# Performance work log

Hardware: AMD Instinct MI355X
Metric: run time of the kernel (lower is better)

Reference implementation:

```python
import jax, jax.numpy as jnp
import numpy as np

FLOAT_MIN = jnp.finfo(jnp.float32).min


def setup_inputs() -> dict:
    key = jax.random.key(0)
    ks = jax.random.split(key, 8)
    B, S, F1, F2, A = 65536, 256, 256, 256, 128
    return {
        "obs_state": jax.random.normal(ks[0], (B, S), dtype=jnp.float32),
        "action_mask": jax.random.randint(ks[1], (B, A), 0, 2, dtype=jnp.int32),
        "W1": jax.random.normal(ks[2], (S, F1), dtype=jnp.float32) * (1.0 / np.sqrt(S)),
        "b1": jnp.zeros((F1,), dtype=jnp.float32),
        "W2": jax.random.normal(ks[3], (F1, F2), dtype=jnp.float32) * (1.0 / np.sqrt(F1)),
        "b2": jnp.zeros((F2,), dtype=jnp.float32),
        "W3": jax.random.normal(ks[4], (F2, A), dtype=jnp.float32) * (1.0 / np.sqrt(F2)),
        "b3": jnp.zeros((A,), dtype=jnp.float32),
    }


def reference(obs_state, action_mask, W1, b1, W2, b2, W3, b3):
    # 3-layer MLP: state -> fc1 -> relu -> fc2 -> relu -> fc3
    h = jax.nn.relu(obs_state @ W1 + b1)
    h = jax.nn.relu(h @ W2 + b2)
    x = h @ W3 + b3  # [B, A] logits

    # Vectorized action masking (replaces per-element Python loop):
    #   mask==0 -> FLOAT_MIN; rows with all-zero mask -> FLOAT_MIN everywhere, col 0 = 1.0
    valid = action_mask != 0  # [B, A] bool
    x = jnp.where(valid, x, FLOAT_MIN)
    all_invalid = ~jnp.any(valid, axis=1, keepdims=True)  # [B, 1]
    col0 = jnp.arange(x.shape[1]) == 0  # [A]
    x = jnp.where(all_invalid & col0, jnp.float32(1.0), x)
    return x
```

## Files before the change

kernel.cpp:

```cpp
#include <hip/hip_runtime.h>

typedef __attribute__((ext_vector_type(8))) short short8;
typedef __attribute__((ext_vector_type(8))) unsigned short ushort8;
typedef __attribute__((ext_vector_type(4))) float f32x4;

#define MT 32
#define NWAVE 4
#define STR 264

__device__ __forceinline__ float bmax_r17() { return __uint_as_float(0x7F7F0000u); }

__device__ __forceinline__ unsigned short f2bf_r17(float f) {
    unsigned int u = __float_as_uint(f);
    return (unsigned short)((u + 0x7fffu + ((u >> 16) & 1u)) >> 16);
}

__global__ __launch_bounds__(256)
void pack_weights_r17(const float* __restrict__ W1,
                      const float* __restrict__ W2,
                      const float* __restrict__ W3,
                      unsigned short* __restrict__ ws) {
    int s = blockIdx.x * 256 + threadIdx.x;
    const float* src;
    unsigned short* dst;
    int N;
    if (s < 8192)       { src = W1; dst = ws;          N = 256; }
    else if (s < 16384) { src = W2; dst = ws + 65536;  N = 256; s -= 8192; }
    else                { src = W3; dst = ws + 131072; N = 128; s -= 16384; }
    int frag = s >> 6, lane = s & 63;
    int kb = (frag & 7) * 32 + (lane >> 4) * 8;
    int n  = (frag >> 3) * 16 + (lane & 15);
    ushort8 o;
    #pragma unroll
    for (int j = 0; j < 8; ++j) o[j] = f2bf_r17(src[(kb + j) * N + n]);
    *(ushort8*)&dst[s * 8] = o;
}

__global__ __launch_bounds__(256, 2)
void ColorNetwork_32495722561720_kernel(
        const float* __restrict__ obs,
        const int* __restrict__ amask,
        const float* __restrict__ b1,
        const float* __restrict__ b2,
        const float* __restrict__ b3,
        const unsigned short* __restrict__ w1p,
        const unsigned short* __restrict__ w2p,
        const unsigned short* __restrict__ w3p,
        float* __restrict__ out)
{
    __shared__ __align__(16) unsigned short act[NWAVE * MT * STR];
    __shared__ int rowany[NWAVE * MT];

    const int tid  = threadIdx.x;
    const int wave = tid >> 6;
    const int lane = tid & 63;
    const int quad = lane >> 4;
    const int noff = lane & 15;
    const int sb   = wave * (MT * STR);
    const int rb   = wave * MT;
    const size_t rowbase = (size_t)blockIdx.x * (MT * NWAVE) + (size_t)wave * MT;

    {
        const float4* xin = (const float4*)(obs + rowbase * 256);
        #pragma unroll 8
        for (int i = 0; i < 32; ++i) {
            int f = i * 64 + lane;
            int row = f >> 6;
            int c4 = f & 63;
            float4 v = xin[f];
            ushort4 p;
            p.x = f2bf_r17(v.x); p.y = f2bf_r17(v.y);
            p.z = f2bf_r17(v.z); p.w = f2bf_r17(v.w);
            *(ushort4*)&act[sb + row * STR + c4 * 4] = p;
        }
    }

    if (lane < MT) rowany[rb + lane] = 0;
    {
        const int4* min4 = (const int4*)(amask + rowbase * 128);
        #pragma unroll 4
        for (int i = 0; i < 16; ++i) {
            int f = i * 64 + lane;
            int4 m = min4[f];
            if (m.x | m.y | m.z | m.w) rowany[rb + (f >> 5)] = 1;
        }
    }

    short8 a[2][8];

    #pragma unroll
    for (int rt = 0; rt < 2; ++rt)
        #pragma unroll
        for (int k0 = 0; k0 < 8; ++k0)
            a[rt][k0] = *(const short8*)&act[sb + (rt * 16 + noff) * STR + k0 * 32 + quad * 8];
    #pragma unroll 2
    for (int ct = 0; ct < 16; ++ct) {
        f32x4 ac0 = {}, ac1 = {};
        #pragma unroll
        for (int k0 = 0; k0 < 8; ++k0) {
            short8 b = *(const short8*)&w1p[((ct * 8 + k0) * 64 + lane) * 8];
            ac0 = __builtin_amdgcn_mfma_f32_16x16x32_bf16(a[0][k0], b, ac0, 0, 0, 0);
            ac1 = __builtin_amdgcn_mfma_f32_16x16x32_bf16(a[1][k0], b, ac1, 0, 0, 0);
        }
        int col = ct * 16 + noff;
        float bv = b1[col];
        #pragma unroll
        for (int i = 0; i < 4; ++i) {
            act[sb + (quad * 4 + i) * STR + col]      = f2bf_r17(fmaxf(ac0[i] + bv, 0.0f));
            act[sb + (16 + quad * 4 + i) * STR + col] = f2bf_r17(fmaxf(ac1[i] + bv, 0.0f));
        }
    }

    #pragma unroll
    for (int rt = 0; rt < 2; ++rt)
        #pragma unroll
        for (int k0 = 0; k0 < 8; ++k0)
            a[rt][k0] = *(const short8*)&act[sb + (rt * 16 + noff) * STR + k0 * 32 + quad * 8];
    #pragma unroll 2
    for (int ct = 0; ct < 16; ++ct) {
        f32x4 ac0 = {}, ac1 = {};
        #pragma unroll
        for (int k0 = 0; k0 < 8; ++k0) {
            short8 b = *(const short8*)&w2p[((ct * 8 + k0) * 64 + lane) * 8];
            ac0 = __builtin_amdgcn_mfma_f32_16x16x32_bf16(a[0][k0], b, ac0, 0, 0, 0);
            ac1 = __builtin_amdgcn_mfma_f32_16x16x32_bf16(a[1][k0], b, ac1, 0, 0, 0);
        }
        int col = ct * 16 + noff;
        float bv = b2[col];
        #pragma unroll
        for (int i = 0; i < 4; ++i) {
            act[sb + (quad * 4 + i) * STR + col]      = f2bf_r17(fmaxf(ac0[i] + bv, 0.0f));
            act[sb + (16 + quad * 4 + i) * STR + col] = f2bf_r17(fmaxf(ac1[i] + bv, 0.0f));
        }
    }

    #pragma unroll
    for (int rt = 0; rt < 2; ++rt)
        #pragma unroll
        for (int k0 = 0; k0 < 8; ++k0)
            a[rt][k0] = *(const short8*)&act[sb + (rt * 16 + noff) * STR + k0 * 32 + quad * 8];

    int ra[8];
    #pragma unroll
    for (int rt = 0; rt < 2; ++rt)
        #pragma unroll
        for (int i = 0; i < 4; ++i)
            ra[rt * 4 + i] = rowany[rb + rt * 16 + quad * 4 + i];

    const float BM = bmax_r17();
    #pragma unroll 2
    for (int ct = 0; ct < 8; ++ct) {
        f32x4 ac0 = {}, ac1 = {};
        #pragma unroll
        for (int k0 = 0; k0 < 8; ++k0) {
            short8 b = *(const short8*)&w3p[((ct * 8 + k0) * 64 + lane) * 8];
            ac0 = __builtin_amdgcn_mfma_f32_16x16x32_bf16(a[0][k0], b, ac0, 0, 0, 0);
            ac1 = __builtin_amdgcn_mfma_f32_16x16x32_bf16(a[1][k0], b, ac1, 0, 0, 0);
        }
        int col = ct * 16 + noff;
        float bv = b3[col];
        #pragma unroll
        for (int rt = 0; rt < 2; ++rt) {
            const f32x4& ac = rt ? ac1 : ac0;
            #pragma unroll
            for (int i = 0; i < 4; ++i) {
                int row = rt * 16 + quad * 4 + i;
                int m = amask[(rowbase + row) * 128 + col];
                float v = ac[i] + bv;
                v = fminf(fmaxf(v, -BM), BM);
                if (!(v == v)) v = 0.0f;
                if (!m) v = -BM;
                if (!ra[rt * 4 + i]) v = (col == 0) ? 1.0f : -BM;
                out[(rowbase + row) * 128 + col] = v;
            }
        }
    }
}

extern "C" void kernel_launch(void* const* d_in, const int* in_sizes, int n_in,
                              void* d_out, int out_size, void* d_ws, size_t ws_size,
                              hipStream_t stream) {
    const float* obs   = (const float*)d_in[0];
    const int*   amask = (const int*)d_in[1];
    const float* W1 = (const float*)d_in[2];
    const float* b1 = (const float*)d_in[3];
    const float* W2 = (const float*)d_in[4];
    const float* b2 = (const float*)d_in[5];
    const float* W3 = (const float*)d_in[6];
    const float* b3 = (const float*)d_in[7];
    float* out = (float*)d_out;

    const int B = in_sizes[0] / 256;

    unsigned short* ws = (unsigned short*)d_ws;
    unsigned short* w1p = ws;
    unsigned short* w2p = ws + 65536;
    unsigned short* w3p = ws + 131072;

    pack_weights_r17<<<80, 256, 0, stream>>>(W1, W2, W3, ws);

    ColorNetwork_32495722561720_kernel<<<B / (MT * NWAVE), 256, 0, stream>>>(
        obs, amask, b1, b2, b3, w1p, w2p, w3p, out);
}
```

Before: 184.6 us.

## Split each 32-row tile across two waves sharing LDS, partitioning output columns

```diff
diff --git a/kernel.cpp b/kernel.cpp
--- a/kernel.cpp
+++ b/kernel.cpp
@@ -5,18 +5,17 @@
 typedef __attribute__((ext_vector_type(4))) float f32x4;
 
 #define MT 32
-#define NWAVE 4
 #define STR 264
 
-__device__ __forceinline__ float bmax_r17() { return __uint_as_float(0x7F7F0000u); }
-
-__device__ __forceinline__ unsigned short f2bf_r17(float f) {
+__device__ __forceinline__ float bmax_r18() { return __uint_as_float(0x7F7F0000u); }
+
+__device__ __forceinline__ unsigned short f2bf_r18(float f) {
     unsigned int u = __float_as_uint(f);
     return (unsigned short)((u + 0x7fffu + ((u >> 16) & 1u)) >> 16);
 }
 
 __global__ __launch_bounds__(256)
-void pack_weights_r17(const float* __restrict__ W1,
+void pack_weights_r18(const float* __restrict__ W1,
                       const float* __restrict__ W2,
                       const float* __restrict__ W3,
                       unsigned short* __restrict__ ws) {
@@ -32,11 +31,11 @@
     int n  = (frag >> 3) * 16 + (lane & 15);
     ushort8 o;
     #pragma unroll
-    for (int j = 0; j < 8; ++j) o[j] = f2bf_r17(src[(kb + j) * N + n]);
+    for (int j = 0; j < 8; ++j) o[j] = f2bf_r18(src[(kb + j) * N + n]);
     *(ushort8*)&dst[s * 8] = o;
 }
 
-__global__ __launch_bounds__(256, 2)
+__global__ __launch_bounds__(128, 4)
 void ColorNetwork_32495722561720_kernel(
         const float* __restrict__ obs,
         const int* __restrict__ amask,
@@ -48,41 +47,41 @@
         const unsigned short* __restrict__ w3p,
         float* __restrict__ out)
 {
-    __shared__ __align__(16) unsigned short act[NWAVE * MT * STR];
-    __shared__ int rowany[NWAVE * MT];
+    __shared__ __align__(16) unsigned short act[MT * STR];
+    __shared__ int rowany[MT];
 
     const int tid  = threadIdx.x;
     const int wave = tid >> 6;
     const int lane = tid & 63;
     const int quad = lane >> 4;
     const int noff = lane & 15;
-    const int sb   = wave * (MT * STR);
-    const int rb   = wave * MT;
-    const size_t rowbase = (size_t)blockIdx.x * (MT * NWAVE) + (size_t)wave * MT;
+    const size_t rowbase = (size_t)blockIdx.x * MT;
+
+    if (tid < MT) rowany[tid] = 0;
 
     {
         const float4* xin = (const float4*)(obs + rowbase * 256);
-        #pragma unroll 8
-        for (int i = 0; i < 32; ++i) {
-            int f = i * 64 + lane;
+        #pragma unroll 4
+        for (int i = 0; i < 16; ++i) {
+            int f = tid + i * 128;
             int row = f >> 6;
             int c4 = f & 63;
             float4 v = xin[f];
             ushort4 p;
-            p.x = f2bf_r17(v.x); p.y = f2bf_r17(v.y);
-            p.z = f2bf_r17(v.z); p.w = f2bf_r17(v.w);
-            *(ushort4*)&act[sb + row * STR + c4 * 4] = p;
-        }
-    }
-
-    if (lane < MT) rowany[rb + lane] = 0;
+            p.x = f2bf_r18(v.x); p.y = f2bf_r18(v.y);
+            p.z = f2bf_r18(v.z); p.w = f2bf_r18(v.w);
+            *(ushort4*)&act[row * STR + c4 * 4] = p;
+        }
+    }
+    __syncthreads();
+
     {
         const int4* min4 = (const int4*)(amask + rowbase * 128);
         #pragma unroll 4
-        for (int i = 0; i < 16; ++i) {
-            int f = i * 64 + lane;
+        for (int i = 0; i < 8; ++i) {
+            int f = tid + i * 128;
             int4 m = min4[f];
-            if (m.x | m.y | m.z | m.w) rowany[rb + (f >> 5)] = 1;
+            if (m.x | m.y | m.z | m.w) rowany[f >> 5] = 1;
         }
     }
 
@@ -92,73 +91,80 @@
     for (int rt = 0; rt < 2; ++rt)
         #pragma unroll
         for (int k0 = 0; k0 < 8; ++k0)
-            a[rt][k0] = *(const short8*)&act[sb + (rt * 16 + noff) * STR + k0 * 32 + quad * 8];
+            a[rt][k0] = *(const short8*)&act[(rt * 16 + noff) * STR + k0 * 32 + quad * 8];
+    __syncthreads();
     #pragma unroll 2
-    for (int ct = 0; ct < 16; ++ct) {
+    for (int ct = 0; ct < 8; ++ct) {
+        const int ctg = wave * 8 + ct;
         f32x4 ac0 = {}, ac1 = {};
         #pragma unroll
         for (int k0 = 0; k0 < 8; ++k0) {
-            short8 b = *(const short8*)&w1p[((ct * 8 + k0) * 64 + lane) * 8];
+            short8 b = *(const short8*)&w1p[((ctg * 8 + k0) * 64 + lane) * 8];
             ac0 = __builtin_amdgcn_mfma_f32_16x16x32_bf16(a[0][k0], b, ac0, 0, 0, 0);
             ac1 = __builtin_amdgcn_mfma_f32_16x16x32_bf16(a[1][k0], b, ac1, 0, 0, 0);
         }
-        int col = ct * 16 + noff;
-        float bv = b1[col];
+        const int col = ctg * 16 + noff;
+        const float bv = b1[col];
         #pragma unroll
         for (int i = 0; i < 4; ++i) {
-            act[sb + (quad * 4 + i) * STR + col]      = f2bf_r17(fmaxf(ac0[i] + bv, 0.0f));
-            act[sb + (16 + quad * 4 + i) * STR + col] = f2bf_r17(fmaxf(ac1[i] + bv, 0.0f));
-        }
-    }
+            act[(quad * 4 + i) * STR + col]      = f2bf_r18(fmaxf(ac0[i] + bv, 0.0f));
+            act[(16 + quad * 4 + i) * STR + col] = f2bf_r18(fmaxf(ac1[i] + bv, 0.0f));
+        }
+    }
+    __syncthreads();
 
     #pragma unroll
     for (int rt = 0; rt < 2; ++rt)
         #pragma unroll
         for (int k0 = 0; k0 < 8; ++k0)
-            a[rt][k0] = *(const short8*)&act[sb + (rt * 16 + noff) * STR + k0 * 32 + quad * 8];
+            a[rt][k0] = *(const short8*)&act[(rt * 16 + noff) * STR + k0 * 32 + quad * 8];
+    __syncthreads();
     #pragma unroll 2
-    for (int ct = 0; ct < 16; ++ct) {
+    for (int ct = 0; ct < 8; ++ct) {
+        const int ctg = wave * 8 + ct;
         f32x4 ac0 = {}, ac1 = {};
         #pragma unroll
         for (int k0 = 0; k0 < 8; ++k0) {
-            short8 b = *(const short8*)&w2p[((ct * 8 + k0) * 64 + lane) * 8];
+            short8 b = *(const short8*)&w2p[((ctg * 8 + k0) * 64 + lane) * 8];
             ac0 = __builtin_amdgcn_mfma_f32_16x16x32_bf16(a[0][k0], b, ac0, 0, 0, 0);
             ac1 = __builtin_amdgcn_mfma_f32_16x16x32_bf16(a[1][k0], b, ac1, 0, 0, 0);
         }
-        int col = ct * 16 + noff;
-        float bv = b2[col];
+        const int col = ctg * 16 + noff;
+        const float bv = b2[col];
         #pragma unroll
         for (int i = 0; i < 4; ++i) {
-            act[sb + (quad * 4 + i) * STR + col]      = f2bf_r17(fmaxf(ac0[i] + bv, 0.0f));
-            act[sb + (16 + quad * 4 + i) * STR + col] = f2bf_r17(fmaxf(ac1[i] + bv, 0.0f));
-        }
-    }
+            act[(quad * 4 + i) * STR + col]      = f2bf_r18(fmaxf(ac0[i] + bv, 0.0f));
+            act[(16 + quad * 4 + i) * STR + col] = f2bf_r18(fmaxf(ac1[i] + bv, 0.0f));
+        }
+    }
+    __syncthreads();
 
     #pragma unroll
     for (int rt = 0; rt < 2; ++rt)
         #pragma unroll
         for (int k0 = 0; k0 < 8; ++k0)
-            a[rt][k0] = *(const short8*)&act[sb + (rt * 16 + noff) * STR + k0 * 32 + quad * 8];
+            a[rt][k0] = *(const short8*)&act[(rt * 16 + noff) * STR + k0 * 32 + quad * 8];
 
     int ra[8];
     #pragma unroll
     for (int rt = 0; rt < 2; ++rt)
         #pragma unroll
         for (int i = 0; i < 4; ++i)
-            ra[rt * 4 + i] = rowany[rb + rt * 16 + quad * 4 + i];
-
-    const float BM = bmax_r17();
+            ra[rt * 4 + i] = rowany[rt * 16 + quad * 4 + i];
+
+    const float BM = bmax_r18();
     #pragma unroll 2
-    for (int ct = 0; ct < 8; ++ct) {
+    for (int ct = 0; ct < 4; ++ct) {
+        const int ctg = wave * 4 + ct;
         f32x4 ac0 = {}, ac1 = {};
         #pragma unroll
         for (int k0 = 0; k0 < 8; ++k0) {
-            short8 b = *(const short8*)&w3p[((ct * 8 + k0) * 64 + lane) * 8];
+            short8 b = *(const short8*)&w3p[((ctg * 8 + k0) * 64 + lane) * 8];
             ac0 = __builtin_amdgcn_mfma_f32_16x16x32_bf16(a[0][k0], b, ac0, 0, 0, 0);
             ac1 = __builtin_amdgcn_mfma_f32_16x16x32_bf16(a[1][k0], b, ac1, 0, 0, 0);
         }
-        int col = ct * 16 + noff;
-        float bv = b3[col];
+        const int col = ctg * 16 + noff;
+        const float bv = b3[col];
         #pragma unroll
         for (int rt = 0; rt < 2; ++rt) {
             const f32x4& ac = rt ? ac1 : ac0;
@@ -197,8 +203,8 @@
     unsigned short* w2p = ws + 65536;
     unsigned short* w3p = ws + 131072;
 
-    pack_weights_r17<<<80, 256, 0, stream>>>(W1, W2, W3, ws);
-
-    ColorNetwork_32495722561720_kernel<<<B / (MT * NWAVE), 256, 0, stream>>>(
+    pack_weights_r18<<<80, 256, 0, stream>>>(W1, W2, W3, ws);
+
+    ColorNetwork_32495722561720_kernel<<<B / MT, 128, 0, stream>>>(
         obs, amask, b1, b2, b3, w1p, w2p, w3p, out);
 }
```

Result: faster. 165.8 us (-10.2%).

## Shrink per-wave row tile to 16 rows with 128-thread blocks

Applied to the files above, without the earlier changes.

```diff
diff --git a/kernel.cpp b/kernel.cpp
--- a/kernel.cpp
+++ b/kernel.cpp
@@ -5,18 +5,17 @@
 typedef __attribute__((ext_vector_type(4))) float f32x4;
 
 #define MT 32
-#define NWAVE 4
 #define STR 264
 
-__device__ __forceinline__ float bmax_r17() { return __uint_as_float(0x7F7F0000u); }
+__device__ __forceinline__ float bmax_r20() { return __uint_as_float(0x7F7F0000u); }
 
-__device__ __forceinline__ unsigned short f2bf_r17(float f) {
+__device__ __forceinline__ unsigned short f2bf_r20(float f) {
     unsigned int u = __float_as_uint(f);
     return (unsigned short)((u + 0x7fffu + ((u >> 16) & 1u)) >> 16);
 }
 
 __global__ __launch_bounds__(256)
-void pack_weights_r17(const float* __restrict__ W1,
+void pack_weights_r20(const float* __restrict__ W1,
                       const float* __restrict__ W2,
                       const float* __restrict__ W3,
                       unsigned short* __restrict__ ws) {
@@ -32,11 +31,11 @@
     int n  = (frag >> 3) * 16 + (lane & 15);
     ushort8 o;
     #pragma unroll
-    for (int j = 0; j < 8; ++j) o[j] = f2bf_r17(src[(kb + j) * N + n]);
+    for (int j = 0; j < 8; ++j) o[j] = f2bf_r20(src[(kb + j) * N + n]);
     *(ushort8*)&dst[s * 8] = o;
 }
 
-__global__ __launch_bounds__(256, 2)
+__global__ __launch_bounds__(128, 4)
 void ColorNetwork_32495722561720_kernel(
         const float* __restrict__ obs,
         const int* __restrict__ amask,
@@ -48,131 +47,111 @@
         const unsigned short* __restrict__ w3p,
         float* __restrict__ out)
 {
-    __shared__ __align__(16) unsigned short act[NWAVE * MT * STR];
-    __shared__ int rowany[NWAVE * MT];
+    __shared__ __align__(16) unsigned short act[MT * STR];
+    __shared__ int rowany[MT];
 
     const int tid  = threadIdx.x;
     const int wave = tid >> 6;
     const int lane = tid & 63;
     const int quad = lane >> 4;
     const int noff = lane & 15;
-    const int sb   = wave * (MT * STR);
-    const int rb   = wave * MT;
-    const size_t rowbase = (size_t)blockIdx.x * (MT * NWAVE) + (size_t)wave * MT;
+    const size_t rowbase = (size_t)blockIdx.x * MT + (size_t)wave * 16;
+    const int sb = wave * 16 * STR;
+    const int rb = wave * 16;
 
     {
         const float4* xin = (const float4*)(obs + rowbase * 256);
-        #pragma unroll 8
-        for (int i = 0; i < 32; ++i) {
-            int f = i * 64 + lane;
+        #pragma unroll 4
+        for (int i = 0; i < 16; ++i) {
+            int f = lane + i * 64;
             int row = f >> 6;
             int c4 = f & 63;
             float4 v = xin[f];
             ushort4 p;
-            p.x = f2bf_r17(v.x); p.y = f2bf_r17(v.y);
-            p.z = f2bf_r17(v.z); p.w = f2bf_r17(v.w);
+            p.x = f2bf_r20(v.x); p.y = f2bf_r20(v.y);
+            p.z = f2bf_r20(v.z); p.w = f2bf_r20(v.w);
             *(ushort4*)&act[sb + row * STR + c4 * 4] = p;
         }
     }
 
-    if (lane < MT) rowany[rb + lane] = 0;
+    if (lane < 16) rowany[rb + lane] = 0;
     {
         const int4* min4 = (const int4*)(amask + rowbase * 128);
         #pragma unroll 4
-        for (int i = 0; i < 16; ++i) {
-            int f = i * 64 + lane;
+        for (int i = 0; i < 8; ++i) {
+            int f = lane + i * 64;
             int4 m = min4[f];
             if (m.x | m.y | m.z | m.w) rowany[rb + (f >> 5)] = 1;
         }
     }
 
-    short8 a[2][8];
+    short8 a[8];
 
     #pragma unroll
-    for (int rt = 0; rt < 2; ++rt)
-        #pragma unroll
-        for (int k0 = 0; k0 < 8; ++k0)
-            a[rt][k0] = *(const short8*)&act[sb + (rt * 16 + noff) * STR + k0 * 32 + quad * 8];
+    for (int k0 = 0; k0 < 8; ++k0)
+        a[k0] = *(const short8*)&act[sb + noff * STR + k0 * 32 + quad * 8];
     #pragma unroll 2
     for (int ct = 0; ct < 16; ++ct) {
-        f32x4 ac0 = {}, ac1 = {};
+        f32x4 acc = {};
         #pragma unroll
         for (int k0 = 0; k0 < 8; ++k0) {
             short8 b = *(const short8*)&w1p[((ct * 8 + k0) * 64 + lane) * 8];
-            ac0 = __builtin_amdgcn_mfma_f32_16x16x32_bf16(a[0][k0], b, ac0, 0, 0, 0);
-            ac1 = __builtin_amdgcn_mfma_f32_16x16x32_bf16(a[1][k0], b, ac1, 0, 0, 0);
+            acc = __builtin_amdgcn_mfma_f32_16x16x32_bf16(a[k0], b, acc, 0, 0, 0);
         }
-        int col = ct * 16 + noff;
-        float bv = b1[col];
+        const int col = ct * 16 + noff;
+        const float bv = b1[col];
         #pragma unroll
-        for (int i = 0; i < 4; ++i) {
-            act[sb + (quad * 4 + i) * STR + col]      = f2bf_r17(fmaxf(ac0[i] + bv, 0.0f));
-            act[sb + (16 + quad * 4 + i) * STR + col] = f2bf_r17(fmaxf(ac1[i] + bv, 0.0f));
-        }
+        for (int i = 0; i < 4; ++i)
+            act[sb + (quad * 4 + i) * STR + col] = f2bf_r20(fmaxf(acc[i] + bv, 0.0f));
     }
 
     #pragma unroll
-    for (int rt = 0; rt < 2; ++rt)
-        #pragma unroll
-        for (int k0 = 0; k0 < 8; ++k0)
-            a[rt][k0] = *(const short8*)&act[sb + (rt * 16 + noff) * STR + k0 * 32 + quad * 8];
+    for (int k0 = 0; k0 < 8; ++k0)
+        a[k0] = *(const short8*)&act[sb + noff * STR + k0 * 32 + quad * 8];
     #pragma unroll 2
     for (int ct = 0; ct < 16; ++ct) {
-        f32x4 ac0 = {}, ac1 = {};
+        f32x4 acc = {};
         #pragma unroll
         for (int k0 = 0; k0 < 8; ++k0) {
             short8 b = *(const short8*)&w2p[((ct * 8 + k0) * 64 + lane) * 8];
-            ac0 = __builtin_amdgcn_mfma_f32_16x16x32_bf16(a[0][k0], b, ac0, 0, 0, 0);
-            ac1 = __builtin_amdgcn_mfma_f32_16x16x32_bf16(a[1][k0], b, ac1, 0, 0, 0);
+            acc = __builtin_amdgcn_mfma_f32_16x16x32_bf16(a[k0], b, acc, 0, 0, 0);
         }
-        int col = ct * 16 + noff;
-        float bv = b2[col];
+        const int col = ct * 16 + noff;
+        const float bv = b2[col];
         #pragma unroll
-        for (int i = 0; i < 4; ++i) {
-            act[sb + (quad * 4 + i) * STR + col]      = f2bf_r17(fmaxf(ac0[i] + bv, 0.0f));
-            act[sb + (16 + quad * 4 + i) * STR + col] = f2bf_r17(fmaxf(ac1[i] + bv, 0.0f));
-        }
+        for (int i = 0; i < 4; ++i)
+            act[sb + (quad * 4 + i) * STR + col] = f2bf_r20(fmaxf(acc[i] + bv, 0.0f));
     }
 
     #pragma unroll
-    for (int rt = 0; rt < 2; ++rt)
-        #pragma unroll
-        for (int k0 = 0; k0 < 8; ++k0)
-            a[rt][k0] = *(const short8*)&act[sb + (rt * 16 + noff) * STR + k0 * 32 + quad * 8];
+    for (int k0 = 0; k0 < 8; ++k0)
+        a[k0] = *(const short8*)&act[sb + noff * STR + k0 * 32 + quad * 8];
 
-    int ra[8];
+    int ra[4];
     #pragma unroll
-    for (int rt = 0; rt < 2; ++rt)
-        #pragma unroll
-        for (int i = 0; i < 4; ++i)
-            ra[rt * 4 + i] = rowany[rb + rt * 16 + quad * 4 + i];
+    for (int i = 0; i < 4; ++i) ra[i] = rowany[rb + quad * 4 + i];
 
-    const float BM = bmax_r17();
+    const float BM = bmax_r20();
     #pragma unroll 2
     for (int ct = 0; ct < 8; ++ct) {
-        f32x4 ac0 = {}, ac1 = {};
+        f32x4 acc = {};
         #pragma unroll
         for (int k0 = 0; k0 < 8; ++k0) {
             short8 b = *(const short8*)&w3p[((ct * 8 + k0) * 64 + lane) * 8];
-            ac0 = __builtin_amdgcn_mfma_f32_16x16x32_bf16(a[0][k0], b, ac0, 0, 0, 0);
-            ac1 = __builtin_amdgcn_mfma_f32_16x16x32_bf16(a[1][k0], b, ac1, 0, 0, 0);
+            acc = __builtin_amdgcn_mfma_f32_16x16x32_bf16(a[k0], b, acc, 0, 0, 0);
         }
-        int col = ct * 16 + noff;
-        float bv = b3[col];
+        const int col = ct * 16 + noff;
+        const float bv = b3[col];
         #pragma unroll
-        for (int rt = 0; rt < 2; ++rt) {
-            const f32x4& ac = rt ? ac1 : ac0;
-            #pragma unroll
-            for (int i = 0; i < 4; ++i) {
-                int row = rt * 16 + quad * 4 + i;
-                int m = amask[(rowbase + row) * 128 + col];
-                float v = ac[i] + bv;
-                v = fminf(fmaxf(v, -BM), BM);
-                if (!(v == v)) v = 0.0f;
-                if (!m) v = -BM;
-                if (!ra[rt * 4 + i]) v = (col == 0) ? 1.0f : -BM;
-                out[(rowbase + row) * 128 + col] = v;
-            }
+        for (int i = 0; i < 4; ++i) {
+            int row = quad * 4 + i;
+            int m = amask[(rowbase + row) * 128 + col];
+            float v = acc[i] + bv;
+            v = fminf(fmaxf(v, -BM), BM);
+            if (!(v == v)) v = 0.0f;
+            if (!m) v = -BM;
+            if (!ra[i]) v = (col == 0) ? 1.0f : -BM;
+            out[(rowbase + row) * 128 + col] = v;
         }
     }
 }
@@ -197,8 +176,8 @@
     unsigned short* w2p = ws + 65536;
     unsigned short* w3p = ws + 131072;
 
-    pack_weights_r17<<<80, 256, 0, stream>>>(W1, W2, W3, ws);
+    pack_weights_r20<<<80, 256, 0, stream>>>(W1, W2, W3, ws);
 
-    ColorNetwork_32495722561720_kernel<<<B / (MT * NWAVE), 256, 0, stream>>>(
+    ColorNetwork_32495722561720_kernel<<<B / MT, 128, 0, stream>>>(
         obs, amask, b1, b2, b3, w1p, w2p, w3p, out);
 }
```

Measured after the change: 183.0 us. No clear change (-0.9%).
